# Kernel tuning notes

Measured on AMD Instinct MI355X. Metric: run time of the kernel, lower is better.

Reference implementation:

```python
import jax, jax.numpy as jnp
import numpy as np

B, S, F, EMB, HID = 64, 2048, 40, 128, 256


def setup_inputs() -> dict:
    key = jax.random.key(0)
    ks = jax.random.split(key, 12)
    sc_in = 1.0 / np.sqrt(F)
    sc_h = 1.0 / np.sqrt(HID)
    n = lambda k, shape, sc: (jax.random.normal(k, shape, jnp.float32) * sc)
    return {
        "in_states": jax.random.normal(ks[0], (B, S, F), jnp.float32),
        "W_in": n(ks[1], (EMB, F), sc_in),
        "b_in": jnp.zeros((EMB,), jnp.float32),  # bias init to 0 in original
        "W_ih0": n(ks[2], (4 * HID, EMB), sc_h),
        "W_hh0": n(ks[3], (4 * HID, HID), sc_h),
        "b_ih0": n(ks[4], (4 * HID,), sc_h),
        "b_hh0": n(ks[5], (4 * HID,), sc_h),
        "W_ih1": n(ks[6], (4 * HID, HID), sc_h),
        "W_hh1": n(ks[7], (4 * HID, HID), sc_h),
        "b_ih1": n(ks[8], (4 * HID,), sc_h),
        "b_hh1": n(ks[9], (4 * HID,), sc_h),
        "W_out": n(ks[10], (1, HID), sc_h),
        "b_out": jnp.zeros((1,), jnp.float32),  # bias init to 0 in original
    }


def _lstm_layer(x, W_ih, W_hh, b_ih, b_hh):
    # x: [B, S, D_in]; returns hs: [B, S, H], final (h, c)
    Bb = x.shape[0]
    H = W_hh.shape[1]
    # Precompute input contribution for all timesteps (one big GEMM).
    gx = jnp.einsum('bsd,gd->bsg', x, W_ih) + b_ih + b_hh  # [B, S, 4H]

    def step(carry, gxt):
        h, c = carry
        g = gxt + h @ W_hh.T  # [B, 4H]
        i, f, gg, o = jnp.split(g, 4, axis=-1)  # PyTorch gate order i,f,g,o
        i = jax.nn.sigmoid(i)
        f = jax.nn.sigmoid(f)
        gg = jnp.tanh(gg)
        o = jax.nn.sigmoid(o)
        c = f * c + i * gg
        h = o * jnp.tanh(c)
        return (h, c), h

    init = (jnp.zeros((Bb, H), x.dtype), jnp.zeros((Bb, H), x.dtype))
    (h, c), hs = jax.lax.scan(step, init, jnp.swapaxes(gx, 0, 1))
    return jnp.swapaxes(hs, 0, 1), (h, c)


def reference(in_states, W_in, b_in, W_ih0, W_hh0, b_ih0, b_hh0,
              W_ih1, W_hh1, b_ih1, b_hh1, W_out, b_out):
    # Input projection applied to every timestep (equivalent to per-step Linear).
    x = jnp.einsum('bsf,ef->bse', in_states, W_in) + b_in  # [B, S, EMB]
    y, _ = _lstm_layer(x, W_ih0, W_hh0, b_ih0, b_hh0)
    y, _ = _lstm_layer(y, W_ih1, W_hh1, b_ih1, b_hh1)
    out = jnp.einsum('bsh,oh->bso', y, W_out) + b_out  # [B, S, 1]
    return out[..., 0]  # [B, S], matches torch.t(outputs)
```

## Files before the change

### kernel.cpp

```cpp
#include <hip/hip_runtime.h>


#define Sz    2048
#define PIPE  4
#define NG    4
#define NJ    8

typedef __attribute__((ext_vector_type(8))) short short8;
typedef __attribute__((ext_vector_type(4))) float f32x4;

#define PUB0_U64 0
#define PUB1_U64 65536
#define CFLG_U32 262144
#define WS_U32   262176

#define HA_HI 0
#define HA_LO 8448
#define HB_HI 16896
#define HB_LO 25344
#define IN_HI 33792
#define IN_LO 36096
#define GBUF  38400
#define SMEM_BYTES 46848
#define WCOMB_OFF 16896

__device__ __forceinline__ unsigned short bf16_rne(float f) {
  unsigned u = __float_as_uint(f);
  u += 0x7FFFu + ((u >> 16) & 1u);
  return (unsigned short)(u >> 16);
}
__device__ __forceinline__ float sigm(float x) { return 1.f / (1.f + __expf(-x)); }
__device__ __forceinline__ float tanh_f(float x) { return 1.f - 2.f / (__expf(2.f * x) + 1.f); }

__device__ __forceinline__ bool load_stage(const unsigned long long* __restrict__ src,
                                           unsigned tagExp, char* hi, char* lo, int tid) {
  unsigned long long v[16];
#pragma unroll
  for (int kt = 0; kt < 8; ++kt) {
    v[kt * 2]     = __hip_atomic_load(src + kt * 512 + tid,       __ATOMIC_RELAXED, __HIP_MEMORY_SCOPE_AGENT);
    v[kt * 2 + 1] = __hip_atomic_load(src + kt * 512 + 256 + tid, __ATOMIC_RELAXED, __HIP_MEMORY_SCOPE_AGENT);
  }
  bool ok = true;
#pragma unroll
  for (int kt = 0; kt < 8; ++kt) {
#pragma unroll
    for (int hh = 0; hh < 2; ++hh) {
      unsigned long long x = v[kt * 2 + hh];
      ok &= ((unsigned)(x >> 32) == tagExp);
      unsigned pk = (unsigned)x;
      int e = tid + hh * 256;
      int m = e >> 5, col = kt * 32 + (e & 31);
      *(short*)(hi + m * 528 + col * 2) = (short)(pk >> 16);
      *(short*)(lo + m * 528 + col * 2) = (short)(pk & 0xffffu);
    }
  }
  return ok;
}

__global__ void zero_kernel(unsigned* __restrict__ ws, float* __restrict__ out) {
  int i = blockIdx.x * 256 + threadIdx.x;
  if (i < WS_U32) ws[i] = 0u;
  if (i < 64 * Sz) out[i] = 0.f;
}

__global__ __launch_bounds__(256, 1) void lstm_persist(
    const float* __restrict__ xin, const float* __restrict__ W_in,
    const float* __restrict__ b_in, const float* __restrict__ W_ih0,
    const float* __restrict__ W_hh0, const float* __restrict__ b_ih0,
    const float* __restrict__ b_hh0, const float* __restrict__ W_ih1,
    const float* __restrict__ W_hh1, const float* __restrict__ b_ih1,
    const float* __restrict__ b_hh1, const float* __restrict__ W_out,
    const float* __restrict__ b_out, float* __restrict__ out,
    unsigned* __restrict__ ws) {
  const int bx = blockIdx.x;
  const int g = bx & 7;
  if (g >= NG) return;
  const int idx = bx >> 3;
  const int layer = idx >> 3;
  const int p = idx & 7;
  const int tid = (int)threadIdx.x;
  const int w = tid >> 6;
  const int lane = tid & 63;
  const int q = lane >> 4;
  const int n16 = lane & 15;

  __shared__ __align__(16) char smem[SMEM_BYTES];

  const int row0 = w * 256 + p * 32 + n16;
  const int row1 = row0 + 16;

  short8 wf_rec[8][2];
  short8 wf_in2[8][2];
  short8 wf_cmb[2][2];
  float bias0 = 0.f, bias1 = 0.f;

  {
    const float* Wrec = layer ? W_hh1 : W_hh0;
#pragma unroll
    for (int kt = 0; kt < 8; ++kt) {
#pragma unroll
      for (int u = 0; u < 2; ++u) {
        const int row = u ? row1 : row0;
        const float* src = Wrec + (size_t)row * 256 + kt * 32 + q * 8;
        union { short8 v; unsigned short s[8]; } fr;
#pragma unroll
        for (int j = 0; j < 8; ++j) fr.s[j] = bf16_rne(src[j]);
        wf_rec[kt][u] = fr.v;
      }
    }
  }
  if (layer == 1) {
#pragma unroll
    for (int kt = 0; kt < 8; ++kt) {
#pragma unroll
      for (int u = 0; u < 2; ++u) {
        const int row = u ? row1 : row0;
        const float* src = W_ih1 + (size_t)row * 256 + kt * 32 + q * 8;
        union { short8 v; unsigned short s[8]; } fr;
#pragma unroll
        for (int j = 0; j < 8; ++j) fr.s[j] = bf16_rne(src[j]);
        wf_in2[kt][u] = fr.v;
      }
    }
    bias0 = b_ih1[row0] + b_hh1[row0];
    bias1 = b_ih1[row1] + b_hh1[row1];
  } else {
    float* wcomb = (float*)(smem + WCOMB_OFF);
    for (int i = tid; i < 128 * 40; i += 256) {
      int rl = i / 40, f = i - rl * 40;
      int gate = rl >> 5, rr = rl & 31;
      int arow = gate * 256 + p * 32 + rr;
      const float* wi = W_ih0 + (size_t)arow * 128;
      float s = 0.f;
      for (int e = 0; e < 128; ++e) s += wi[e] * W_in[e * 40 + f];
      wcomb[rl * 40 + f] = s;
    }
    __syncthreads();
#pragma unroll
    for (int kt = 0; kt < 2; ++kt) {
#pragma unroll
      for (int u = 0; u < 2; ++u) {
        int rl = w * 32 + u * 16 + n16;
        union { short8 v; unsigned short s[8]; } fr;
#pragma unroll
        for (int j = 0; j < 8; ++j) {
          int k = kt * 32 + q * 8 + j;
          fr.s[j] = (k < 40) ? bf16_rne(wcomb[rl * 40 + k]) : (unsigned short)0;
        }
        wf_cmb[kt][u] = fr.v;
      }
    }
    {
      const float* wi0 = W_ih0 + (size_t)row0 * 128;
      const float* wi1 = W_ih0 + (size_t)row1 * 128;
      float s0 = 0.f, s1 = 0.f;
      for (int e = 0; e < 128; ++e) { s0 += wi0[e] * b_in[e]; s1 += wi1[e] * b_in[e]; }
      bias0 = s0 + b_ih0[row0] + b_hh0[row0];
      bias1 = s1 + b_ih0[row1] + b_hh0[row1];
    }
    __syncthreads();
    for (int i = tid; i < 2304; i += 256) *((short*)(smem + IN_HI) + i) = 0;
    __syncthreads();
  }

  float c0 = 0.f, c1 = 0.f;
  float wo = 0.f, bo = 0.f;
  if (layer == 1) { wo = W_out[p * 32 + (tid & 31)]; bo = b_out[0]; }

  unsigned long long* const pub0 = (unsigned long long*)ws + PUB0_U64;
  unsigned long long* const pub1 = (unsigned long long*)ws + PUB1_U64;
  unsigned long long* const pubMy = layer ? pub1 : pub0;
  unsigned* const cflg = ws + CFLG_U32 + g * 8;
  float* gb = (float*)(smem + GBUF);

#pragma unroll 1
  for (int t = 0; t < Sz; ++t) {
    if (layer == 0 && tid < 160) {
      int bb = tid / 10, f4 = tid - bb * 10;
      float4 inv = *(const float4*)(xin + ((size_t)(g * 16 + bb) * Sz + t) * 40 + f4 * 4);
#pragma unroll
      for (int cc = 0; cc < 4; ++cc) {
        float f = ((const float*)&inv)[cc];
        unsigned short hb = bf16_rne(f);
        float fh = __uint_as_float((unsigned)hb << 16);
        unsigned short lb = bf16_rne(f - fh);
        int col = f4 * 4 + cc;
        *(short*)(smem + IN_HI + bb * 144 + col * 2) = (short)hb;
        *(short*)(smem + IN_LO + bb * 144 + col * 2) = (short)lb;
      }
    }

    const int slot_r = (t + PIPE - 1) % PIPE;
    const unsigned long long* srcA = pubMy + (size_t)((g * PIPE + slot_r) * NJ) * 512;
    const unsigned long long* srcB = pub0 + (size_t)((g * PIPE + (t % PIPE)) * NJ) * 512;
    const unsigned tagA = (unsigned)t;
    const unsigned tagB = (unsigned)(t + 1);
    for (;;) {
      bool ok = load_stage(srcA, tagA, smem + HA_HI, smem + HA_LO, tid);
      if (layer == 1) {
        ok &= load_stage(srcB, tagB, smem + HB_HI, smem + HB_LO, tid);
      } else if (tid < 8) {
        unsigned c = __hip_atomic_load(cflg + tid, __ATOMIC_RELAXED, __HIP_MEMORY_SCOPE_AGENT);
        ok &= ((int)c >= t - 3);
      }
      if (__syncthreads_and(ok)) break;
    }
    if (layer == 1 && tid == 0)
      __hip_atomic_store(cflg + p, (unsigned)(t + 1), __ATOMIC_RELAXED, __HIP_MEMORY_SCOPE_AGENT);

    f32x4 acc0 = {0.f, 0.f, 0.f, 0.f};
    f32x4 acc1 = {0.f, 0.f, 0.f, 0.f};
    const int arow = n16 * 528;
    const int kcol = q * 8;
#pragma unroll
    for (int kt = 0; kt < 8; ++kt) {
      short8 aH = *(const short8*)(smem + HA_HI + arow + (kt * 32 + kcol) * 2);
      short8 aL = *(const short8*)(smem + HA_LO + arow + (kt * 32 + kcol) * 2);
      acc0 = __builtin_amdgcn_mfma_f32_16x16x32_bf16(aH, wf_rec[kt][0], acc0, 0, 0, 0);
      acc0 = __builtin_amdgcn_mfma_f32_16x16x32_bf16(aL, wf_rec[kt][0], acc0, 0, 0, 0);
      acc1 = __builtin_amdgcn_mfma_f32_16x16x32_bf16(aH, wf_rec[kt][1], acc1, 0, 0, 0);
      acc1 = __builtin_amdgcn_mfma_f32_16x16x32_bf16(aL, wf_rec[kt][1], acc1, 0, 0, 0);
    }
    if (layer == 1) {
#pragma unroll
      for (int kt = 0; kt < 8; ++kt) {
        short8 aH = *(const short8*)(smem + HB_HI + arow + (kt * 32 + kcol) * 2);
        short8 aL = *(const short8*)(smem + HB_LO + arow + (kt * 32 + kcol) * 2);
        acc0 = __builtin_amdgcn_mfma_f32_16x16x32_bf16(aH, wf_in2[kt][0], acc0, 0, 0, 0);
        acc0 = __builtin_amdgcn_mfma_f32_16x16x32_bf16(aL, wf_in2[kt][0], acc0, 0, 0, 0);
        acc1 = __builtin_amdgcn_mfma_f32_16x16x32_bf16(aH, wf_in2[kt][1], acc1, 0, 0, 0);
        acc1 = __builtin_amdgcn_mfma_f32_16x16x32_bf16(aL, wf_in2[kt][1], acc1, 0, 0, 0);
      }
    } else {
      const int arow_in = n16 * 144;
#pragma unroll
      for (int kt = 0; kt < 2; ++kt) {
        short8 aH = *(const short8*)(smem + IN_HI + arow_in + (kt * 32 + kcol) * 2);
        short8 aL = *(const short8*)(smem + IN_LO + arow_in + (kt * 32 + kcol) * 2);
        acc0 = __builtin_amdgcn_mfma_f32_16x16x32_bf16(aH, wf_cmb[kt][0], acc0, 0, 0, 0);
        acc0 = __builtin_amdgcn_mfma_f32_16x16x32_bf16(aL, wf_cmb[kt][0], acc0, 0, 0, 0);
        acc1 = __builtin_amdgcn_mfma_f32_16x16x32_bf16(aH, wf_cmb[kt][1], acc1, 0, 0, 0);
        acc1 = __builtin_amdgcn_mfma_f32_16x16x32_bf16(aL, wf_cmb[kt][1], acc1, 0, 0, 0);
      }
    }

#pragma unroll
    for (int u = 0; u < 2; ++u) {
      f32x4 a = u ? acc1 : acc0;
      float bs = u ? bias1 : bias0;
#pragma unroll
      for (int r = 0; r < 4; ++r) {
        float v = a[r] + bs;
        v = (w == 2) ? tanh_f(v) : sigm(v);
        gb[w * 528 + (q * 4 + r) * 33 + u * 16 + n16] = v;
      }
    }
    __syncthreads();

    unsigned long long* dst =
        pubMy + (size_t)((g * PIPE + (t % PIPE)) * NJ + p) * 512;
    const unsigned long long tagW = ((unsigned long long)(unsigned)(t + 1)) << 32;
#pragma unroll
    for (int k = 0; k < 2; ++k) {
      int e = tid + k * 256;
      int m = e >> 5, nn = e & 31;
      float iv = gb[0 * 528 + m * 33 + nn];
      float fv = gb[1 * 528 + m * 33 + nn];
      float gv = gb[2 * 528 + m * 33 + nn];
      float ov = gb[3 * 528 + m * 33 + nn];
      float c = k ? c1 : c0;
      c = fv * c + iv * gv;
      float h = ov * tanh_f(c);
      if (k) c1 = c; else c0 = c;
      unsigned short hb = bf16_rne(h);
      float fh = __uint_as_float((unsigned)hb << 16);
      unsigned short lb = bf16_rne(h - fh);
      unsigned pk = ((unsigned)hb << 16) | (unsigned)lb;
      __hip_atomic_store(dst + e, tagW | pk, __ATOMIC_RELAXED, __HIP_MEMORY_SCOPE_AGENT);
      if (layer == 1) {
        float val = h * wo;
#pragma unroll
        for (int off = 16; off; off >>= 1) val += __shfl_down(val, off, 32);
        if (nn == 0) {
          if (p == 0) val += bo;
          atomicAdd(out + (size_t)(g * 16 + m) * Sz + t, val);
        }
      }
    }
  }
}

extern "C" void kernel_launch(void* const* d_in, const int* in_sizes, int n_in,
                              void* d_out, int out_size, void* d_ws, size_t ws_size,
                              hipStream_t stream) {
  const float* xin   = (const float*)d_in[0];
  const float* W_in  = (const float*)d_in[1];
  const float* b_in  = (const float*)d_in[2];
  const float* W_ih0 = (const float*)d_in[3];
  const float* W_hh0 = (const float*)d_in[4];
  const float* b_ih0 = (const float*)d_in[5];
  const float* b_hh0 = (const float*)d_in[6];
  const float* W_ih1 = (const float*)d_in[7];
  const float* W_hh1 = (const float*)d_in[8];
  const float* b_ih1 = (const float*)d_in[9];
  const float* b_hh1 = (const float*)d_in[10];
  const float* W_out = (const float*)d_in[11];
  const float* b_out = (const float*)d_in[12];
  float* out = (float*)d_out;
  unsigned* ws = (unsigned*)d_ws;

  zero_kernel<<<(WS_U32 + 255) / 256, 256, 0, stream>>>(ws, out);
  lstm_persist<<<128, 256, 0, stream>>>(xin, W_in, b_in, W_ih0, W_hh0, b_ih0, b_hh0,
                                        W_ih1, W_hh1, b_ih1, b_hh1, W_out, b_out,
                                        out, ws);
}
```

Measured before the change: 7.578 ms.

## Restructure persistent LSTM into three-role pipeline with half-hidden blocks

Replaces the 64-block layer-by-slice persistent kernel with 24 blocks of 512 threads in three roles: layer-0 recurrence, layer-1 input projection (W_ih1 applied to layer-0 h), and layer-1 recurrence. Each batch group's hidden state is split across two blocks, so per-step exchange traffic and cross-block barrier fan-in drop. Each block keeps its own half of h locally in LDS, computes all four gates in registers via lane shuffles instead of an LDS gate buffer, and prefetches the next input. The output dot product is accumulated per block and finished in a separate reduction kernel instead of global atomics. The risks are a deeper ring with new polling and backoff logic, and more MFMA work per block on the serial critical path.

Measured after the change: 19.44 ms. 2.57x slower.

```diff
diff --git a/kernel.cpp b/kernel.cpp
--- a/kernel.cpp
+++ b/kernel.cpp
@@ -1,291 +1,454 @@
 #include <hip/hip_runtime.h>
 
 
-#define Sz    2048
-#define PIPE  4
-#define NG    4
-#define NJ    8
+#define Sz 2048
 
 typedef __attribute__((ext_vector_type(8))) short short8;
 typedef __attribute__((ext_vector_type(4))) float f32x4;
 
-#define PUB0_U64 0
-#define PUB1_U64 65536
-#define CFLG_U32 262144
-#define WS_U32   262176
+#define H1_BASE 131072
+#define IX_BASE 196608
+#define CF_WORD 1441792
+#define GH_WORD 1441824
+#define ZERO_WORDS 1441824
 
 #define HA_HI 0
 #define HA_LO 8448
-#define HB_HI 16896
-#define HB_LO 25344
-#define IN_HI 33792
-#define IN_LO 36096
-#define GBUF  38400
-#define SMEM_BYTES 46848
-#define WCOMB_OFF 16896
+#define IN_HI 16896
+#define IN_LO 19200
+#define POUT_LDS 16896
+#define SMEM_BYTES 21504
 
 __device__ __forceinline__ unsigned short bf16_rne(float f) {
   unsigned u = __float_as_uint(f);
   u += 0x7FFFu + ((u >> 16) & 1u);
   return (unsigned short)(u >> 16);
 }
+__device__ __forceinline__ unsigned pk_enc(float f) {
+  unsigned short hb = bf16_rne(f);
+  float fh = __uint_as_float((unsigned)hb << 16);
+  unsigned short lb = bf16_rne(f - fh);
+  return ((unsigned)hb << 16) | (unsigned)lb;
+}
+__device__ __forceinline__ float pk_dec(unsigned p) {
+  return __uint_as_float(p & 0xffff0000u) + __uint_as_float(p << 16);
+}
 __device__ __forceinline__ float sigm(float x) { return 1.f / (1.f + __expf(-x)); }
 __device__ __forceinline__ float tanh_f(float x) { return 1.f - 2.f / (__expf(2.f * x) + 1.f); }
-
-__device__ __forceinline__ bool load_stage(const unsigned long long* __restrict__ src,
-                                           unsigned tagExp, char* hi, char* lo, int tid) {
-  unsigned long long v[16];
-#pragma unroll
-  for (int kt = 0; kt < 8; ++kt) {
-    v[kt * 2]     = __hip_atomic_load(src + kt * 512 + tid,       __ATOMIC_RELAXED, __HIP_MEMORY_SCOPE_AGENT);
-    v[kt * 2 + 1] = __hip_atomic_load(src + kt * 512 + 256 + tid, __ATOMIC_RELAXED, __HIP_MEMORY_SCOPE_AGENT);
-  }
+__device__ __forceinline__ f32x4 xor8(f32x4 v) {
+  f32x4 r;
+  r[0] = __shfl_xor(v[0], 8, 64); r[1] = __shfl_xor(v[1], 8, 64);
+  r[2] = __shfl_xor(v[2], 8, 64); r[3] = __shfl_xor(v[3], 8, 64);
+  return r;
+}
+
+__device__ __forceinline__ bool stage_half(const unsigned long long* __restrict__ src,
+                                           unsigned tagExp, int dhalf, int tid, char* smem) {
   bool ok = true;
 #pragma unroll
-  for (int kt = 0; kt < 8; ++kt) {
-#pragma unroll
-    for (int hh = 0; hh < 2; ++hh) {
-      unsigned long long x = v[kt * 2 + hh];
-      ok &= ((unsigned)(x >> 32) == tagExp);
-      unsigned pk = (unsigned)x;
-      int e = tid + hh * 256;
-      int m = e >> 5, col = kt * 32 + (e & 31);
-      *(short*)(hi + m * 528 + col * 2) = (short)(pk >> 16);
-      *(short*)(lo + m * 528 + col * 2) = (short)(pk & 0xffffu);
-    }
+  for (int k2 = 0; k2 < 4; ++k2) {
+    unsigned long long x = __hip_atomic_load(src + k2 * 512 + tid,
+                                             __ATOMIC_RELAXED, __HIP_MEMORY_SCOPE_AGENT);
+    ok &= ((unsigned)(x >> 32) == tagExp);
+    int e = k2 * 512 + tid;
+    int m = e >> 7, c = dhalf * 128 + (e & 127);
+    unsigned p = (unsigned)x;
+    *(short*)(smem + HA_HI + m * 528 + c * 2) = (short)(p >> 16);
+    *(short*)(smem + HA_LO + m * 528 + c * 2) = (short)(p & 0xffffu);
   }
   return ok;
 }
 
-__global__ void zero_kernel(unsigned* __restrict__ ws, float* __restrict__ out) {
-  int i = blockIdx.x * 256 + threadIdx.x;
-  if (i < WS_U32) ws[i] = 0u;
-  if (i < 64 * Sz) out[i] = 0.f;
-}
-
-__global__ __launch_bounds__(256, 1) void lstm_persist(
+__global__ void zero_ws(unsigned* __restrict__ ws) {
+  int i = blockIdx.x * 512 + threadIdx.x;
+  if (i < ZERO_WORDS) ws[i] = 0u;
+}
+
+__global__ void out_reduce(const unsigned* __restrict__ ws,
+                           const float* __restrict__ b_out, float* __restrict__ out) {
+  int idx = blockIdx.x * 512 + threadIdx.x;
+  if (idx >= 64 * Sz) return;
+  int b = idx >> 11, t = idx & 2047;
+  int g = b >> 4, m = b & 15;
+  const float* gh = (const float*)(ws + GH_WORD);
+  out[idx] = b_out[0] + gh[((size_t)(g * 2 + 0) * Sz + t) * 16 + m]
+                      + gh[((size_t)(g * 2 + 1) * Sz + t) * 16 + m];
+}
+
+__global__ __launch_bounds__(512, 2) void lstm_v3(
     const float* __restrict__ xin, const float* __restrict__ W_in,
     const float* __restrict__ b_in, const float* __restrict__ W_ih0,
     const float* __restrict__ W_hh0, const float* __restrict__ b_ih0,
     const float* __restrict__ b_hh0, const float* __restrict__ W_ih1,
     const float* __restrict__ W_hh1, const float* __restrict__ b_ih1,
     const float* __restrict__ b_hh1, const float* __restrict__ W_out,
-    const float* __restrict__ b_out, float* __restrict__ out,
-    unsigned* __restrict__ ws) {
+    const float* __restrict__ b_out, unsigned* __restrict__ ws) {
   const int bx = blockIdx.x;
-  const int g = bx & 7;
-  if (g >= NG) return;
-  const int idx = bx >> 3;
-  const int layer = idx >> 3;
-  const int p = idx & 7;
+  if (bx >= 24) return;
+  const int role = bx >> 3;
+  const int gh = bx & 7;
+  const int g = gh >> 1, h = gh & 1;
   const int tid = (int)threadIdx.x;
   const int w = tid >> 6;
   const int lane = tid & 63;
   const int q = lane >> 4;
   const int n16 = lane & 15;
+  const int n3 = n16 & 7;
+  const int hf = n16 >> 3;
 
   __shared__ __align__(16) char smem[SMEM_BYTES];
 
-  const int row0 = w * 256 + p * 32 + n16;
-  const int row1 = row0 + 16;
-
-  short8 wf_rec[8][2];
-  short8 wf_in2[8][2];
-  short8 wf_cmb[2][2];
-  float bias0 = 0.f, bias1 = 0.f;
-
-  {
-    const float* Wrec = layer ? W_hh1 : W_hh0;
-#pragma unroll
-    for (int kt = 0; kt < 8; ++kt) {
-#pragma unroll
-      for (int u = 0; u < 2; ++u) {
-        const int row = u ? row1 : row0;
+  unsigned long long* const ring = (unsigned long long*)ws;
+  unsigned* const cfm = ws + CF_WORD;
+  unsigned* const cfc = ws + CF_WORD + 8;
+  float* const ghout = (float*)(ws + GH_WORD);
+  float* const pout = (float*)(smem + POUT_LDS);
+
+  short8 wf[2][2][8];
+  const float* Wrec = (role == 0) ? W_hh0 : (role == 1) ? W_ih1 : W_hh1;
+#pragma unroll
+  for (int j = 0; j < 2; ++j)
+#pragma unroll
+    for (int u = 0; u < 2; ++u) {
+      const int row = (u * 2 + hf) * 256 + h * 128 + w * 16 + j * 8 + n3;
+#pragma unroll
+      for (int kt = 0; kt < 8; ++kt) {
         const float* src = Wrec + (size_t)row * 256 + kt * 32 + q * 8;
         union { short8 v; unsigned short s[8]; } fr;
 #pragma unroll
-        for (int j = 0; j < 8; ++j) fr.s[j] = bf16_rne(src[j]);
-        wf_rec[kt][u] = fr.v;
-      }
-    }
-  }
-  if (layer == 1) {
-#pragma unroll
-    for (int kt = 0; kt < 8; ++kt) {
+        for (int z = 0; z < 8; ++z) fr.s[z] = bf16_rne(src[z]);
+        wf[j][u][kt] = fr.v;
+      }
+    }
+
+  short8 wfc[2][2][2];
+  float b8[2][4];
+  float bias4[2][2];
+  float wo[2] = {0.f, 0.f};
+  if (role == 0) {
+#pragma unroll
+    for (int j = 0; j < 2; ++j)
 #pragma unroll
       for (int u = 0; u < 2; ++u) {
-        const int row = u ? row1 : row0;
-        const float* src = W_ih1 + (size_t)row * 256 + kt * 32 + q * 8;
-        union { short8 v; unsigned short s[8]; } fr;
-#pragma unroll
-        for (int j = 0; j < 8; ++j) fr.s[j] = bf16_rne(src[j]);
-        wf_in2[kt][u] = fr.v;
-      }
-    }
-    bias0 = b_ih1[row0] + b_hh1[row0];
-    bias1 = b_ih1[row1] + b_hh1[row1];
+        const int row = (u * 2 + hf) * 256 + h * 128 + w * 16 + j * 8 + n3;
+        const float* wr = W_ih0 + (size_t)row * 128;
+        float s0[8] = {0, 0, 0, 0, 0, 0, 0, 0};
+        float s1[8] = {0, 0, 0, 0, 0, 0, 0, 0};
+        for (int e = 0; e < 128; ++e) {
+          float wv = wr[e];
+          const float* wi = W_in + e * 40;
+#pragma unroll
+          for (int z = 0; z < 8; ++z) s0[z] += wv * wi[q * 8 + z];
+          if (q == 0) {
+#pragma unroll
+            for (int z = 0; z < 8; ++z) s1[z] += wv * wi[32 + z];
+          }
+        }
+        union { short8 v; unsigned short s[8]; } f0, f1;
+#pragma unroll
+        for (int z = 0; z < 8; ++z) {
+          f0.s[z] = bf16_rne(s0[z]);
+          f1.s[z] = (q == 0) ? bf16_rne(s1[z]) : (unsigned short)0;
+        }
+        wfc[j][u][0] = f0.v;
+        wfc[j][u][1] = f1.v;
+      }
+#pragma unroll
+    for (int j = 0; j < 2; ++j) {
+      const int colg = h * 128 + w * 16 + j * 8 + n3;
+#pragma unroll
+      for (int G = 0; G < 4; ++G) {
+        const int row = G * 256 + colg;
+        float s = b_ih0[row] + b_hh0[row];
+        const float* wr = W_ih0 + (size_t)row * 128;
+        for (int e = 0; e < 128; ++e) s += wr[e] * b_in[e];
+        b8[j][G] = s;
+      }
+    }
+  } else if (role == 1) {
+#pragma unroll
+    for (int j = 0; j < 2; ++j)
+#pragma unroll
+      for (int u = 0; u < 2; ++u) {
+        const int row = (u * 2 + hf) * 256 + h * 128 + w * 16 + j * 8 + n3;
+        bias4[j][u] = b_ih1[row] + b_hh1[row];
+      }
   } else {
-    float* wcomb = (float*)(smem + WCOMB_OFF);
-    for (int i = tid; i < 128 * 40; i += 256) {
-      int rl = i / 40, f = i - rl * 40;
-      int gate = rl >> 5, rr = rl & 31;
-      int arow = gate * 256 + p * 32 + rr;
-      const float* wi = W_ih0 + (size_t)arow * 128;
+#pragma unroll
+    for (int j = 0; j < 2; ++j) wo[j] = W_out[h * 128 + w * 16 + j * 8 + n3];
+  }
+
+  for (int i = tid; i < 4224; i += 512) ((int*)smem)[i] = 0;
+  if (role == 0)
+    for (int i = tid; i < 1152; i += 512) ((int*)(smem + IN_HI))[i] = 0;
+  __syncthreads();
+  if (role == 0 && tid < 160) {
+    int bb = tid / 10, f4 = tid - bb * 10;
+    float4 xv = *(const float4*)(xin + ((size_t)(g * 16 + bb) * Sz) * 40 + f4 * 4);
+#pragma unroll
+    for (int cc = 0; cc < 4; ++cc) {
+      float f = ((const float*)&xv)[cc];
+      unsigned p = pk_enc(f);
+      int col = f4 * 4 + cc;
+      *(short*)(smem + IN_HI + bb * 144 + col * 2) = (short)(p >> 16);
+      *(short*)(smem + IN_LO + bb * 144 + col * 2) = (short)(p & 0xffffu);
+    }
+  }
+
+  float cst[2][2] = {{0.f, 0.f}, {0.f, 0.f}};
+
+  if (role == 0) {
+#pragma unroll 1
+    for (int t = 0; t < Sz; ++t) {
+      float4 xv;
+      const bool hasx = (t + 1 < Sz) && (tid < 160);
+      int bb = 0, f4 = 0;
+      if (hasx) {
+        bb = tid / 10; f4 = tid - bb * 10;
+        xv = *(const float4*)(xin + ((size_t)(g * 16 + bb) * Sz + (t + 1)) * 40 + f4 * 4);
+      }
+      const unsigned long long* srcP =
+          ring + ((size_t)(g * 8 + ((t + 7) & 7)) * 2 + (1 - h)) * 2048;
+      bool okP = false, okM = (tid >= 2);
+      int fails = 0;
+      for (;;) {
+        if (!okP) okP = stage_half(srcP, (unsigned)t, 1 - h, tid, smem);
+        if (!okM) {
+          unsigned c = __hip_atomic_load(cfm + g * 2 + tid, __ATOMIC_RELAXED,
+                                         __HIP_MEMORY_SCOPE_AGENT);
+          okM = ((int)c >= t - 7);
+        }
+        if (__syncthreads_and(okP && okM)) break;
+        if (++fails > 2) __builtin_amdgcn_s_sleep(1);
+      }
+      f32x4 acc[2][2] = {{{0,0,0,0},{0,0,0,0}},{{0,0,0,0},{0,0,0,0}}};
+#pragma unroll
+      for (int kt = 0; kt < 2; ++kt) {
+        short8 aH = *(const short8*)(smem + IN_HI + n16 * 144 + (kt * 32 + q * 8) * 2);
+        short8 aL = *(const short8*)(smem + IN_LO + n16 * 144 + (kt * 32 + q * 8) * 2);
+#pragma unroll
+        for (int j = 0; j < 2; ++j)
+#pragma unroll
+          for (int u = 0; u < 2; ++u) {
+            acc[j][u] = __builtin_amdgcn_mfma_f32_16x16x32_bf16(aH, wfc[j][u][kt], acc[j][u], 0, 0, 0);
+            acc[j][u] = __builtin_amdgcn_mfma_f32_16x16x32_bf16(aL, wfc[j][u][kt], acc[j][u], 0, 0, 0);
+          }
+      }
+#pragma unroll
+      for (int kt = 0; kt < 8; ++kt) {
+        short8 aH = *(const short8*)(smem + HA_HI + n16 * 528 + (kt * 32 + q * 8) * 2);
+        short8 aL = *(const short8*)(smem + HA_LO + n16 * 528 + (kt * 32 + q * 8) * 2);
+#pragma unroll
+        for (int j = 0; j < 2; ++j)
+#pragma unroll
+          for (int u = 0; u < 2; ++u) {
+            acc[j][u] = __builtin_amdgcn_mfma_f32_16x16x32_bf16(aH, wf[j][u][kt], acc[j][u], 0, 0, 0);
+            acc[j][u] = __builtin_amdgcn_mfma_f32_16x16x32_bf16(aL, wf[j][u][kt], acc[j][u], 0, 0, 0);
+          }
+      }
+      __syncthreads();
+      unsigned long long* dst = ring + ((size_t)(g * 8 + (t & 7)) * 2 + h) * 2048;
+      const unsigned long long tagW = ((unsigned long long)(unsigned)(t + 1)) << 32;
+#pragma unroll
+      for (int j = 0; j < 2; ++j) {
+        f32x4 a0 = acc[j][0], a1 = acc[j][1];
+        f32x4 x0 = xor8(a0), x1 = xor8(a1);
+#pragma unroll
+        for (int rs = 0; rs < 2; ++rs) {
+          const int r = hf * 2 + rs;
+          float pi = hf ? x0[r] : a0[r];
+          float pf = hf ? a0[r] : x0[r];
+          float pg = hf ? x1[r] : a1[r];
+          float po = hf ? a1[r] : x1[r];
+          pi = sigm(pi + b8[j][0]); pf = sigm(pf + b8[j][1]);
+          pg = tanh_f(pg + b8[j][2]); po = sigm(po + b8[j][3]);
+          float c = pf * cst[j][rs] + pi * pg;
+          cst[j][rs] = c;
+          float hv = po * tanh_f(c);
+          const int m = q * 4 + r, colL = w * 16 + j * 8 + n3;
+          unsigned p = pk_enc(hv);
+          __hip_atomic_store(dst + m * 128 + colL, tagW | p,
+                             __ATOMIC_RELAXED, __HIP_MEMORY_SCOPE_AGENT);
+          const int cg = h * 128 + colL;
+          *(short*)(smem + HA_HI + m * 528 + cg * 2) = (short)(p >> 16);
+          *(short*)(smem + HA_LO + m * 528 + cg * 2) = (short)(p & 0xffffu);
+        }
+      }
+      if (hasx) {
+#pragma unroll
+        for (int cc = 0; cc < 4; ++cc) {
+          float f = ((const float*)&xv)[cc];
+          unsigned p = pk_enc(f);
+          int col = f4 * 4 + cc;
+          *(short*)(smem + IN_HI + bb * 144 + col * 2) = (short)(p >> 16);
+          *(short*)(smem + IN_LO + bb * 144 + col * 2) = (short)(p & 0xffffu);
+        }
+      }
+    }
+  }
+  else if (role == 1) {
+#pragma unroll 1
+    for (int t = 0; t < Sz; ++t) {
+      const unsigned long long* srcH = ring + ((size_t)(g * 8 + (t & 7)) * 2) * 2048;
+      bool okH = false, okC = (tid != 0);
+      int fails = 0;
+      for (;;) {
+        if (!okH) {
+          bool ok = true;
+#pragma unroll
+          for (int k2 = 0; k2 < 8; ++k2) {
+            unsigned long long x = __hip_atomic_load(srcH + k2 * 512 + tid,
+                                                     __ATOMIC_RELAXED, __HIP_MEMORY_SCOPE_AGENT);
+            ok &= ((unsigned)(x >> 32) == (unsigned)(t + 1));
+            int e = k2 * 512 + tid;
+            int hh = e >> 11, ee = e & 2047;
+            int m = ee >> 7, c = hh * 128 + (ee & 127);
+            unsigned p = (unsigned)x;
+            *(short*)(smem + HA_HI + m * 528 + c * 2) = (short)(p >> 16);
+            *(short*)(smem + HA_LO + m * 528 + c * 2) = (short)(p & 0xffffu);
+          }
+          okH = ok;
+        }
+        if (!okC) {
+          unsigned c = __hip_atomic_load(cfc + gh, __ATOMIC_RELAXED, __HIP_MEMORY_SCOPE_AGENT);
+          okC = ((int)c >= t - 7);
+        }
+        if (__syncthreads_and(okH && okC)) break;
+        if (++fails > 2) __builtin_amdgcn_s_sleep(1);
+      }
+      if (tid == 0)
+        __hip_atomic_store(cfm + gh, (unsigned)(t + 1), __ATOMIC_RELAXED, __HIP_MEMORY_SCOPE_AGENT);
+      f32x4 acc[2][2] = {{{0,0,0,0},{0,0,0,0}},{{0,0,0,0},{0,0,0,0}}};
+#pragma unroll
+      for (int kt = 0; kt < 8; ++kt) {
+        short8 aH = *(const short8*)(smem + HA_HI + n16 * 528 + (kt * 32 + q * 8) * 2);
+        short8 aL = *(const short8*)(smem + HA_LO + n16 * 528 + (kt * 32 + q * 8) * 2);
+#pragma unroll
+        for (int j = 0; j < 2; ++j)
+#pragma unroll
+          for (int u = 0; u < 2; ++u) {
+            acc[j][u] = __builtin_amdgcn_mfma_f32_16x16x32_bf16(aH, wf[j][u][kt], acc[j][u], 0, 0, 0);
+            acc[j][u] = __builtin_amdgcn_mfma_f32_16x16x32_bf16(aL, wf[j][u][kt], acc[j][u], 0, 0, 0);
+          }
+      }
+      __syncthreads();
+      unsigned long long* dst = ring + IX_BASE + ((size_t)(g * 8 + (t & 7)) * 2 + h) * 8192;
+      const unsigned long long tagW = ((unsigned long long)(unsigned)(t + 1)) << 32;
+#pragma unroll
+      for (int j = 0; j < 2; ++j)
+#pragma unroll
+        for (int u = 0; u < 2; ++u) {
+          const int G = u * 2 + hf;
+          const int colL = w * 16 + j * 8 + n3;
+          const float bb = bias4[j][u];
+#pragma unroll
+          for (int r = 0; r < 4; ++r) {
+            float val = acc[j][u][r] + bb;
+            __hip_atomic_store(dst + ((size_t)(G * 128 + colL) * 16 + q * 4 + r),
+                               tagW | pk_enc(val), __ATOMIC_RELAXED, __HIP_MEMORY_SCOPE_AGENT);
+          }
+        }
+    }
+  }
+  else {
+#pragma unroll 1
+    for (int t = 0; t < Sz; ++t) {
+      const unsigned long long* srcP =
+          ring + H1_BASE + ((size_t)(g * 4 + ((t + 3) & 3)) * 2 + (1 - h)) * 2048;
+      const unsigned long long* srcX =
+          ring + IX_BASE + ((size_t)(g * 8 + (t & 7)) * 2 + h) * 8192;
+      bool okP = false, okX = false;
+      int fails = 0;
+      unsigned ixp[4][2][2];
+      for (;;) {
+        if (!okP) okP = stage_half(srcP, (unsigned)t, 1 - h, tid, smem);
+        if (!okX) {
+          bool ok = true;
+#pragma unroll
+          for (int G = 0; G < 4; ++G)
+#pragma unroll
+            for (int j = 0; j < 2; ++j)
+#pragma unroll
+              for (int rs = 0; rs < 2; ++rs) {
+                const size_t word = (size_t)(G * 128 + w * 16 + j * 8 + n3) * 16
+                                    + q * 4 + hf * 2 + rs;
+                unsigned long long x = __hip_atomic_load(srcX + word,
+                                                         __ATOMIC_RELAXED, __HIP_MEMORY_SCOPE_AGENT);
+                ok &= ((unsigned)(x >> 32) == (unsigned)(t + 1));
+                ixp[G][j][rs] = (unsigned)x;
+              }
+          okX = ok;
+        }
+        if (__syncthreads_and(okP && okX)) break;
+        if (++fails > 2) __builtin_amdgcn_s_sleep(1);
+      }
+      if (tid == 0)
+        __hip_atomic_store(cfc + gh, (unsigned)(t + 1), __ATOMIC_RELAXED, __HIP_MEMORY_SCOPE_AGENT);
+      if (w == 0 && lane < 16 && t > 0) {
+        float s = 0.f;
+#pragma unroll
+        for (int ww = 0; ww < 8; ++ww) s += pout[((t - 1) & 1) * 128 + ww * 16 + lane];
+        ghout[((size_t)(g * 2 + h) * Sz + (t - 1)) * 16 + lane] = s;
+      }
+      f32x4 acc[2][2] = {{{0,0,0,0},{0,0,0,0}},{{0,0,0,0},{0,0,0,0}}};
+#pragma unroll
+      for (int kt = 0; kt < 8; ++kt) {
+        short8 aH = *(const short8*)(smem + HA_HI + n16 * 528 + (kt * 32 + q * 8) * 2);
+        short8 aL = *(const short8*)(smem + HA_LO + n16 * 528 + (kt * 32 + q * 8) * 2);
+#pragma unroll
+        for (int j = 0; j < 2; ++j)
+#pragma unroll
+          for (int u = 0; u < 2; ++u) {
+            acc[j][u] = __builtin_amdgcn_mfma_f32_16x16x32_bf16(aH, wf[j][u][kt], acc[j][u], 0, 0, 0);
+            acc[j][u] = __builtin_amdgcn_mfma_f32_16x16x32_bf16(aL, wf[j][u][kt], acc[j][u], 0, 0, 0);
+          }
+      }
+      __syncthreads();
+      unsigned long long* dst = ring + H1_BASE + ((size_t)(g * 4 + (t & 3)) * 2 + h) * 2048;
+      const unsigned long long tagW = ((unsigned long long)(unsigned)(t + 1)) << 32;
+      float vj[2] = {0.f, 0.f};
+#pragma unroll
+      for (int j = 0; j < 2; ++j) {
+        f32x4 a0 = acc[j][0], a1 = acc[j][1];
+        f32x4 x0 = xor8(a0), x1 = xor8(a1);
+#pragma unroll
+        for (int rs = 0; rs < 2; ++rs) {
+          const int r = hf * 2 + rs;
+          float pi = (hf ? x0[r] : a0[r]) + pk_dec(ixp[0][j][rs]);
+          float pf = (hf ? a0[r] : x0[r]) + pk_dec(ixp[1][j][rs]);
+          float pg = (hf ? x1[r] : a1[r]) + pk_dec(ixp[2][j][rs]);
+          float po = (hf ? a1[r] : x1[r]) + pk_dec(ixp[3][j][rs]);
+          pi = sigm(pi); pf = sigm(pf); pg = tanh_f(pg); po = sigm(po);
+          float c = pf * cst[j][rs] + pi * pg;
+          cst[j][rs] = c;
+          float hv = po * tanh_f(c);
+          const int m = q * 4 + r, colL = w * 16 + j * 8 + n3;
+          unsigned p = pk_enc(hv);
+          __hip_atomic_store(dst + m * 128 + colL, tagW | p,
+                             __ATOMIC_RELAXED, __HIP_MEMORY_SCOPE_AGENT);
+          const int cg = h * 128 + colL;
+          *(short*)(smem + HA_HI + m * 528 + cg * 2) = (short)(p >> 16);
+          *(short*)(smem + HA_LO + m * 528 + cg * 2) = (short)(p & 0xffffu);
+          vj[rs] += hv * wo[j];
+        }
+      }
+#pragma unroll
+      for (int msk = 1; msk <= 4; msk <<= 1) {
+        vj[0] += __shfl_xor(vj[0], msk, 64);
+        vj[1] += __shfl_xor(vj[1], msk, 64);
+      }
+      if (n3 == 0) {
+        const int m0 = q * 4 + hf * 2;
+        pout[(t & 1) * 128 + w * 16 + m0] = vj[0];
+        pout[(t & 1) * 128 + w * 16 + m0 + 1] = vj[1];
+      }
+    }
+    __syncthreads();
+    if (w == 0 && lane < 16) {
       float s = 0.f;
-      for (int e = 0; e < 128; ++e) s += wi[e] * W_in[e * 40 + f];
-      wcomb[rl * 40 + f] = s;
-    }
-    __syncthreads();
-#pragma unroll
-    for (int kt = 0; kt < 2; ++kt) {
-#pragma unroll
-      for (int u = 0; u < 2; ++u) {
-        int rl = w * 32 + u * 16 + n16;
-        union { short8 v; unsigned short s[8]; } fr;
-#pragma unroll
-        for (int j = 0; j < 8; ++j) {
-          int k = kt * 32 + q * 8 + j;
-          fr.s[j] = (k < 40) ? bf16_rne(wcomb[rl * 40 + k]) : (unsigned short)0;
-        }
-        wf_cmb[kt][u] = fr.v;
-      }
-    }
-    {
-      const float* wi0 = W_ih0 + (size_t)row0 * 128;
-      const float* wi1 = W_ih0 + (size_t)row1 * 128;
-      float s0 = 0.f, s1 = 0.f;
-      for (int e = 0; e < 128; ++e) { s0 += wi0[e] * b_in[e]; s1 += wi1[e] * b_in[e]; }
-      bias0 = s0 + b_ih0[row0] + b_hh0[row0];
-      bias1 = s1 + b_ih0[row1] + b_hh0[row1];
-    }
-    __syncthreads();
-    for (int i = tid; i < 2304; i += 256) *((short*)(smem + IN_HI) + i) = 0;
-    __syncthreads();
-  }
-
-  float c0 = 0.f, c1 = 0.f;
-  float wo = 0.f, bo = 0.f;
-  if (layer == 1) { wo = W_out[p * 32 + (tid & 31)]; bo = b_out[0]; }
-
-  unsigned long long* const pub0 = (unsigned long long*)ws + PUB0_U64;
-  unsigned long long* const pub1 = (unsigned long long*)ws + PUB1_U64;
-  unsigned long long* const pubMy = layer ? pub1 : pub0;
-  unsigned* const cflg = ws + CFLG_U32 + g * 8;
-  float* gb = (float*)(smem + GBUF);
-
-#pragma unroll 1
-  for (int t = 0; t < Sz; ++t) {
-    if (layer == 0 && tid < 160) {
-      int bb = tid / 10, f4 = tid - bb * 10;
-      float4 inv = *(const float4*)(xin + ((size_t)(g * 16 + bb) * Sz + t) * 40 + f4 * 4);
-#pragma unroll
-      for (int cc = 0; cc < 4; ++cc) {
-        float f = ((const float*)&inv)[cc];
-        unsigned short hb = bf16_rne(f);
-        float fh = __uint_as_float((unsigned)hb << 16);
-        unsigned short lb = bf16_rne(f - fh);
-        int col = f4 * 4 + cc;
-        *(short*)(smem + IN_HI + bb * 144 + col * 2) = (short)hb;
-        *(short*)(smem + IN_LO + bb * 144 + col * 2) = (short)lb;
-      }
-    }
-
-    const int slot_r = (t + PIPE - 1) % PIPE;
-    const unsigned long long* srcA = pubMy + (size_t)((g * PIPE + slot_r) * NJ) * 512;
-    const unsigned long long* srcB = pub0 + (size_t)((g * PIPE + (t % PIPE)) * NJ) * 512;
-    const unsigned tagA = (unsigned)t;
-    const unsigned tagB = (unsigned)(t + 1);
-    for (;;) {
-      bool ok = load_stage(srcA, tagA, smem + HA_HI, smem + HA_LO, tid);
-      if (layer == 1) {
-        ok &= load_stage(srcB, tagB, smem + HB_HI, smem + HB_LO, tid);
-      } else if (tid < 8) {
-        unsigned c = __hip_atomic_load(cflg + tid, __ATOMIC_RELAXED, __HIP_MEMORY_SCOPE_AGENT);
-        ok &= ((int)c >= t - 3);
-      }
-      if (__syncthreads_and(ok)) break;
-    }
-    if (layer == 1 && tid == 0)
-      __hip_atomic_store(cflg + p, (unsigned)(t + 1), __ATOMIC_RELAXED, __HIP_MEMORY_SCOPE_AGENT);
-
-    f32x4 acc0 = {0.f, 0.f, 0.f, 0.f};
-    f32x4 acc1 = {0.f, 0.f, 0.f, 0.f};
-    const int arow = n16 * 528;
-    const int kcol = q * 8;
-#pragma unroll
-    for (int kt = 0; kt < 8; ++kt) {
-      short8 aH = *(const short8*)(smem + HA_HI + arow + (kt * 32 + kcol) * 2);
-      short8 aL = *(const short8*)(smem + HA_LO + arow + (kt * 32 + kcol) * 2);
-      acc0 = __builtin_amdgcn_mfma_f32_16x16x32_bf16(aH, wf_rec[kt][0], acc0, 0, 0, 0);
-      acc0 = __builtin_amdgcn_mfma_f32_16x16x32_bf16(aL, wf_rec[kt][0], acc0, 0, 0, 0);
-      acc1 = __builtin_amdgcn_mfma_f32_16x16x32_bf16(aH, wf_rec[kt][1], acc1, 0, 0, 0);
-      acc1 = __builtin_amdgcn_mfma_f32_16x16x32_bf16(aL, wf_rec[kt][1], acc1, 0, 0, 0);
-    }
-    if (layer == 1) {
-#pragma unroll
-      for (int kt = 0; kt < 8; ++kt) {
-        short8 aH = *(const short8*)(smem + HB_HI + arow + (kt * 32 + kcol) * 2);
-        short8 aL = *(const short8*)(smem + HB_LO + arow + (kt * 32 + kcol) * 2);
-        acc0 = __builtin_amdgcn_mfma_f32_16x16x32_bf16(aH, wf_in2[kt][0], acc0, 0, 0, 0);
-        acc0 = __builtin_amdgcn_mfma_f32_16x16x32_bf16(aL, wf_in2[kt][0], acc0, 0, 0, 0);
-        acc1 = __builtin_amdgcn_mfma_f32_16x16x32_bf16(aH, wf_in2[kt][1], acc1, 0, 0, 0);
-        acc1 = __builtin_amdgcn_mfma_f32_16x16x32_bf16(aL, wf_in2[kt][1], acc1, 0, 0, 0);
-      }
-    } else {
-      const int arow_in = n16 * 144;
-#pragma unroll
-      for (int kt = 0; kt < 2; ++kt) {
-        short8 aH = *(const short8*)(smem + IN_HI + arow_in + (kt * 32 + kcol) * 2);
-        short8 aL = *(const short8*)(smem + IN_LO + arow_in + (kt * 32 + kcol) * 2);
-        acc0 = __builtin_amdgcn_mfma_f32_16x16x32_bf16(aH, wf_cmb[kt][0], acc0, 0, 0, 0);
-        acc0 = __builtin_amdgcn_mfma_f32_16x16x32_bf16(aL, wf_cmb[kt][0], acc0, 0, 0, 0);
-        acc1 = __builtin_amdgcn_mfma_f32_16x16x32_bf16(aH, wf_cmb[kt][1], acc1, 0, 0, 0);
-        acc1 = __builtin_amdgcn_mfma_f32_16x16x32_bf16(aL, wf_cmb[kt][1], acc1, 0, 0, 0);
-      }
-    }
-
-#pragma unroll
-    for (int u = 0; u < 2; ++u) {
-      f32x4 a = u ? acc1 : acc0;
-      float bs = u ? bias1 : bias0;
-#pragma unroll
-      for (int r = 0; r < 4; ++r) {
-        float v = a[r] + bs;
-        v = (w == 2) ? tanh_f(v) : sigm(v);
-        gb[w * 528 + (q * 4 + r) * 33 + u * 16 + n16] = v;
-      }
-    }
-    __syncthreads();
-
-    unsigned long long* dst =
-        pubMy + (size_t)((g * PIPE + (t % PIPE)) * NJ + p) * 512;
-    const unsigned long long tagW = ((unsigned long long)(unsigned)(t + 1)) << 32;
-#pragma unroll
-    for (int k = 0; k < 2; ++k) {
-      int e = tid + k * 256;
-      int m = e >> 5, nn = e & 31;
-      float iv = gb[0 * 528 + m * 33 + nn];
-      float fv = gb[1 * 528 + m * 33 + nn];
-      float gv = gb[2 * 528 + m * 33 + nn];
-      float ov = gb[3 * 528 + m * 33 + nn];
-      float c = k ? c1 : c0;
-      c = fv * c + iv * gv;
-      float h = ov * tanh_f(c);
-      if (k) c1 = c; else c0 = c;
-      unsigned short hb = bf16_rne(h);
-      float fh = __uint_as_float((unsigned)hb << 16);
-      unsigned short lb = bf16_rne(h - fh);
-      unsigned pk = ((unsigned)hb << 16) | (unsigned)lb;
-      __hip_atomic_store(dst + e, tagW | pk, __ATOMIC_RELAXED, __HIP_MEMORY_SCOPE_AGENT);
-      if (layer == 1) {
-        float val = h * wo;
-#pragma unroll
-        for (int off = 16; off; off >>= 1) val += __shfl_down(val, off, 32);
-        if (nn == 0) {
-          if (p == 0) val += bo;
-          atomicAdd(out + (size_t)(g * 16 + m) * Sz + t, val);
-        }
-      }
+#pragma unroll
+      for (int ww = 0; ww < 8; ++ww) s += pout[((Sz - 1) & 1) * 128 + ww * 16 + lane];
+      ghout[((size_t)(g * 2 + h) * Sz + (Sz - 1)) * 16 + lane] = s;
     }
   }
 }
@@ -309,8 +472,8 @@
   float* out = (float*)d_out;
   unsigned* ws = (unsigned*)d_ws;
 
-  zero_kernel<<<(WS_U32 + 255) / 256, 256, 0, stream>>>(ws, out);
-  lstm_persist<<<128, 256, 0, stream>>>(xin, W_in, b_in, W_ih0, W_hh0, b_ih0, b_hh0,
-                                        W_ih1, W_hh1, b_ih1, b_hh1, W_out, b_out,
-                                        out, ws);
-}
+  zero_ws<<<(ZERO_WORDS + 511) / 512, 512, 0, stream>>>(ws);
+  lstm_v3<<<24, 512, 0, stream>>>(xin, W_in, b_in, W_ih0, W_hh0, b_ih0, b_hh0,
+                                  W_ih1, W_hh1, b_ih1, b_hh1, W_out, b_out, ws);
+  out_reduce<<<(64 * Sz + 511) / 512, 512, 0, stream>>>(ws, b_out, out);
+}
```
